# Performance work log

Measured on AMD Instinct MI355X. Metric: run time of the kernel, lower is better.

Reference implementation:

```python
import jax, jax.numpy as jnp
import numpy as np

MARGIN = 0.0
GAP = 0.4
N, D, C = 8192, 128, 10


def setup_inputs() -> dict:
    key = jax.random.key(0)
    k1, k2, k3 = jax.random.split(key, 3)
    inputs = jax.random.normal(k1, (N, D), dtype=jnp.float32)
    pred = jax.random.normal(k2, (N, C), dtype=jnp.float32)
    targets = jax.random.randint(k3, (N,), 0, C, dtype=jnp.int64)
    return {"inputs": inputs, "pred": pred, "targets": targets}


def reference(inputs, pred, targets):
    n = inputs.shape[0]
    # pairwise euclidean distances: ||xi||^2 + ||xj||^2 - 2 xi.xj, clamped + sqrt
    sq = jnp.sum(inputs * inputs, axis=1)                      # [n]
    dist = sq[:, None] + sq[None, :] - 2.0 * (inputs @ inputs.T)
    dist = jnp.sqrt(jnp.clip(dist, 1e-12))                     # [n, n]
    same = targets[:, None] == targets[None, :]                # [n, n] bool

    # confusion detection (original runs under no_grad)
    p = jax.nn.softmax(jax.lax.stop_gradient(pred), axis=1)
    val, top2 = jax.lax.top_k(p, 2)                            # [n,2]
    confuse = (val[:, 0] - val[:, 1] <= GAP) | (top2[:, 0] != targets)  # [n]

    # hard mining per row: hardest positive (max over same-class), hardest negative (min over diff-class)
    dist_ap = jnp.max(jnp.where(same, dist, -jnp.inf), axis=1)  # [n]
    dist_an = jnp.min(jnp.where(same, jnp.inf, dist), axis=1)   # [n]

    # MarginRankingLoss(margin=MARGIN) with y=1: mean(relu(-(an - ap) + margin)) over confused rows
    per_row = jnp.maximum(dist_ap - dist_an + MARGIN, 0.0)
    cnt = jnp.sum(confuse.astype(jnp.float32))
    loss = jnp.sum(jnp.where(confuse, per_row, 0.0)) / jnp.maximum(cnt, 1.0)
    return jnp.where(cnt > 0, loss, 0.0)
```

## Files before the change

kernel.cpp:

```cpp
#include <hip/hip_runtime.h>

#define NROWS 8192
#define DIMX  128
#define DIM2  160
#define NCLS  10
#define GAPV  0.4f
#define BIAS  2048.0f
#define C0    128.0f
#define CHUNK 512
#define NJ    (CHUNK / 16)

typedef __attribute__((ext_vector_type(8))) short bf16x8;
typedef __attribute__((ext_vector_type(4))) float f32x4;

__device__ __forceinline__ unsigned fenc(float f) {
  unsigned u = __float_as_uint(f);
  return (u & 0x80000000u) ? ~u : (u | 0x80000000u);
}
__device__ __forceinline__ float fdec(unsigned u) {
  return (u & 0x80000000u) ? __uint_as_float(u & 0x7fffffffu) : __uint_as_float(~u);
}
__device__ __forceinline__ short f2bf(float f) {
  unsigned u = __float_as_uint(f);
  u += 0x7fffu + ((u >> 16) & 1u);
  return (short)(u >> 16);
}

__global__ __launch_bounds__(256) void prep_k(const float* __restrict__ x,
                                              const int* __restrict__ tgt,
                                              const float* __restrict__ pred,
                                              short* __restrict__ xa,
                                              short* __restrict__ xbm,
                                              float* __restrict__ sq,
                                              unsigned* __restrict__ emax,
                                              unsigned* __restrict__ emin,
                                              int* __restrict__ conf) {
  const int wave = threadIdx.x >> 6;
  const int lane = threadIdx.x & 63;
  const int row  = blockIdx.x * 4 + wave;
  const float* p = x + (size_t)row * DIMX;
  const float a = p[lane];
  const float b = p[lane + 64];
  float s = a * a + b * b;
  #pragma unroll
  for (int m = 1; m < 64; m <<= 1) s += __shfl_xor(s, m, 64);

  short* pa = xa  + (size_t)row * DIM2;
  short* pb = xbm + (size_t)row * DIM2;
  pa[lane] = f2bf(a); pa[lane + 64] = f2bf(b);
  pb[lane] = f2bf(a); pb[lane + 64] = f2bf(b);

  const int cls = tgt[row];
  if (lane < 32) {
    short va, vb;
    if (lane == 0)          { va = (short)0x3F80; vb = f2bf(-0.5f * (s - C0)); }
    else if (lane <= NCLS)  { const bool hit = (lane - 1) == cls;
                              va = hit ? (short)0x4200 : (short)0;
                              vb = hit ? (short)0xC200 : (short)0; }
    else                    { va = 0; vb = 0; }
    pa[128 + lane] = va;
    pb[128 + lane] = vb;
  }

  if (lane == 0) {
    sq[row]   = s;
    emax[row] = fenc(-INFINITY);
    emin[row] = fenc(INFINITY);
    const float* pp = pred + (size_t)row * NCLS;
    float v[NCLS];
    #pragma unroll
    for (int c = 0; c < NCLS; ++c) v[c] = pp[c];
    float m1 = v[0]; int i1 = 0;
    #pragma unroll
    for (int c = 1; c < NCLS; ++c)
      if (v[c] > m1) { m1 = v[c]; i1 = c; }
    float m2 = -INFINITY, sum = 0.f;
    #pragma unroll
    for (int c = 0; c < NCLS; ++c) {
      sum += __expf(v[c] - m1);
      if (c != i1) m2 = fmaxf(m2, v[c]);
    }
    const float d01 = (1.f - __expf(m2 - m1)) / sum;
    conf[row] = (d01 <= GAPV) || (i1 != cls);
  }
}

__global__ __launch_bounds__(64, 2) void gram_k(const short* __restrict__ xa,
                                                const short* __restrict__ xbm,
                                                unsigned* __restrict__ emax,
                                                unsigned* __restrict__ emin) {
  const int lane = threadIdx.x;
  const int quad = lane >> 4;
  const int m16  = lane & 15;
  const int i0    = blockIdx.x * 64;
  const int jbase = blockIdx.y * CHUNK;

  bf16x8 A[4][5];
  #pragma unroll
  for (int r = 0; r < 4; ++r) {
    const short* pa = xa + (size_t)(i0 + r * 16 + m16) * DIM2 + quad * 8;
    #pragma unroll
    for (int ks = 0; ks < 5; ++ks)
      A[r][ks] = *(const bf16x8*)(pa + ks * 32);
  }

  float gmin[4][4], gmax[4][4];
  #pragma unroll
  for (int r = 0; r < 4; ++r)
    #pragma unroll
    for (int q = 0; q < 4; ++q) { gmin[r][q] = INFINITY; gmax[r][q] = -INFINITY; }

  const short* pb0 = xbm + (size_t)(jbase + m16) * DIM2 + quad * 8;
  bf16x8 Bc[5];
  #pragma unroll
  for (int ks = 0; ks < 5; ++ks) Bc[ks] = *(const bf16x8*)(pb0 + ks * 32);

  #pragma unroll 2
  for (int jt = 0; jt < NJ; ++jt) {
    const short* pn = pb0 + (size_t)((jt + 1 < NJ) ? (jt + 1) * 16 : 0) * DIM2;
    bf16x8 Bn[5];
    #pragma unroll
    for (int ks = 0; ks < 5; ++ks) Bn[ks] = *(const bf16x8*)(pn + ks * 32);

    f32x4 acc[4];
    #pragma unroll
    for (int r = 0; r < 4; ++r) acc[r] = (f32x4){0.f, 0.f, 0.f, 0.f};
    #pragma unroll
    for (int ks = 0; ks < 5; ++ks)
      #pragma unroll
      for (int r = 0; r < 4; ++r)
        acc[r] = __builtin_amdgcn_mfma_f32_16x16x32_bf16(A[r][ks], Bc[ks], acc[r], 0, 0, 0);

    #pragma unroll
    for (int r = 0; r < 4; ++r)
      #pragma unroll
      for (int q = 0; q < 4; ++q) {
        gmin[r][q] = fminf(gmin[r][q], acc[r][q]);
        gmax[r][q] = fmaxf(gmax[r][q], acc[r][q]);
      }

    #pragma unroll
    for (int ks = 0; ks < 5; ++ks) Bc[ks] = Bn[ks];
  }

  #pragma unroll
  for (int m = 1; m <= 8; m <<= 1)
    #pragma unroll
    for (int r = 0; r < 4; ++r)
      #pragma unroll
      for (int q = 0; q < 4; ++q) {
        gmin[r][q] = fminf(gmin[r][q], __shfl_xor(gmin[r][q], m, 64));
        gmax[r][q] = fmaxf(gmax[r][q], __shfl_xor(gmax[r][q], m, 64));
      }

  if (m16 == 0) {
    #pragma unroll
    for (int r = 0; r < 4; ++r)
      #pragma unroll
      for (int q = 0; q < 4; ++q) {
        const int row = i0 + r * 16 + quad * 4 + q;
        atomicMax(&emax[row], fenc(C0 - 2.f * gmin[r][q] - BIAS));
        atomicMin(&emin[row], fenc(C0 - 2.f * gmax[r][q]));
      }
  }
}

__global__ __launch_bounds__(1024) void finalize_k(const float* __restrict__ sq,
                                                   const unsigned* __restrict__ emax,
                                                   const unsigned* __restrict__ emin,
                                                   const int* __restrict__ conf,
                                                   float* __restrict__ out) {
  float s = 0.f, c = 0.f;
  for (int row = threadIdx.x; row < NROWS; row += 1024) {
    if (conf[row]) {
      const float ap = sqrtf(fmaxf(sq[row] + fdec(emax[row]), 1e-12f));
      const float an = sqrtf(fmaxf(sq[row] + fdec(emin[row]), 1e-12f));
      s += fmaxf(ap - an, 0.f);
      c += 1.f;
    }
  }
  #pragma unroll
  for (int m = 1; m < 64; m <<= 1) {
    s += __shfl_xor(s, m, 64);
    c += __shfl_xor(c, m, 64);
  }
  __shared__ float ss[16], cc[16];
  const int wid = threadIdx.x >> 6;
  if ((threadIdx.x & 63) == 0) { ss[wid] = s; cc[wid] = c; }
  __syncthreads();
  if (threadIdx.x == 0) {
    float S = 0.f, C = 0.f;
    for (int w = 0; w < 16; ++w) { S += ss[w]; C += cc[w]; }
    out[0] = (C > 0.f) ? (S / fmaxf(C, 1.f)) : 0.f;
  }
}

extern "C" void kernel_launch(void* const* d_in, const int* in_sizes, int n_in,
                              void* d_out, int out_size, void* d_ws, size_t ws_size,
                              hipStream_t stream) {
  const float* x    = (const float*)d_in[0];
  const float* pred = (const float*)d_in[1];
  const int*   tgt  = (const int*)d_in[2];
  float* out = (float*)d_out;

  char* w = (char*)d_ws;
  const size_t arr_bytes = (size_t)NROWS * DIM2 * 2;
  short*    xa   = (short*)w;
  short*    xbm  = (short*)(w + arr_bytes);
  float*    sq   = (float*)(w + 2 * arr_bytes);
  unsigned* emax = (unsigned*)(w + 2 * arr_bytes + (size_t)NROWS * 4);
  unsigned* emin = (unsigned*)(w + 2 * arr_bytes + (size_t)NROWS * 8);
  int*      conf = (int*)(w + 2 * arr_bytes + (size_t)NROWS * 12);

  hipLaunchKernelGGL(prep_k, dim3(NROWS / 4), dim3(256), 0, stream,
                     x, tgt, pred, xa, xbm, sq, emax, emin, conf);
  hipLaunchKernelGGL(gram_k, dim3(NROWS / 64, NROWS / CHUNK), dim3(64), 0, stream,
                     xa, xbm, emax, emin);
  hipLaunchKernelGGL(finalize_k, dim3(1), dim3(1024), 0, stream,
                     sq, emax, emin, conf, out);
}
```

Measured before the change: 99.70 us.

## Share B tiles across four waves via double-buffered LDS staging in gram kernel

```diff
diff --git a/kernel.cpp b/kernel.cpp
--- a/kernel.cpp
+++ b/kernel.cpp
@@ -8,7 +8,9 @@
 #define BIAS  2048.0f
 #define C0    128.0f
 #define CHUNK 512
-#define NJ    (CHUNK / 16)
+#define SLAB  32
+#define NSLAB (CHUNK / SLAB)
+#define LDST  168
 
 typedef __attribute__((ext_vector_type(8))) short bf16x8;
 typedef __attribute__((ext_vector_type(4))) float f32x4;
@@ -85,14 +87,17 @@
   }
 }
 
-__global__ __launch_bounds__(64, 2) void gram_k(const short* __restrict__ xa,
-                                                const short* __restrict__ xbm,
-                                                unsigned* __restrict__ emax,
-                                                unsigned* __restrict__ emin) {
-  const int lane = threadIdx.x;
+__global__ __launch_bounds__(256, 2) void gram_k(const short* __restrict__ xa,
+                                                 const short* __restrict__ xbm,
+                                                 unsigned* __restrict__ emax,
+                                                 unsigned* __restrict__ emin) {
+  __shared__ short lds[2][SLAB * LDST];
+  const int tid  = threadIdx.x;
+  const int wave = tid >> 6;
+  const int lane = tid & 63;
   const int quad = lane >> 4;
   const int m16  = lane & 15;
-  const int i0    = blockIdx.x * 64;
+  const int i0    = blockIdx.x * 256 + wave * 64;
   const int jbase = blockIdx.y * CHUNK;
 
   bf16x8 A[4][5];
@@ -110,37 +115,53 @@
     #pragma unroll
     for (int q = 0; q < 4; ++q) { gmin[r][q] = INFINITY; gmax[r][q] = -INFINITY; }
 
-  const short* pb0 = xbm + (size_t)(jbase + m16) * DIM2 + quad * 8;
-  bf16x8 Bc[5];
-  #pragma unroll
-  for (int ks = 0; ks < 5; ++ks) Bc[ks] = *(const bf16x8*)(pb0 + ks * 32);
-
-  #pragma unroll 2
-  for (int jt = 0; jt < NJ; ++jt) {
-    const short* pn = pb0 + (size_t)((jt + 1 < NJ) ? (jt + 1) * 16 : 0) * DIM2;
-    bf16x8 Bn[5];
-    #pragma unroll
-    for (int ks = 0; ks < 5; ++ks) Bn[ks] = *(const bf16x8*)(pn + ks * 32);
-
-    f32x4 acc[4];
-    #pragma unroll
-    for (int r = 0; r < 4; ++r) acc[r] = (f32x4){0.f, 0.f, 0.f, 0.f};
-    #pragma unroll
-    for (int ks = 0; ks < 5; ++ks)
+  const int scol = tid >> 3;
+  const int sseg = tid & 3 ? (tid & 7) : (tid & 7);
+  uint2 st[5];
+  {
+    const short* g0 = xbm + (size_t)(jbase + scol) * DIM2 + (tid & 7) * 4;
+    #pragma unroll
+    for (int u = 0; u < 5; ++u) st[u] = *(const uint2*)(g0 + u * 32);
+  }
+
+  for (int s = 0; s < NSLAB; ++s) {
+    short* buf = lds[s & 1];
+    {
+      short* dst = buf + scol * LDST + (tid & 7) * 4;
+      #pragma unroll
+      for (int u = 0; u < 5; ++u) *(uint2*)(dst + u * 32) = st[u];
+    }
+    if (s + 1 < NSLAB) {
+      const short* gn = xbm + (size_t)(jbase + (s + 1) * SLAB + scol) * DIM2 + (tid & 7) * 4;
+      #pragma unroll
+      for (int u = 0; u < 5; ++u) st[u] = *(const uint2*)(gn + u * 32);
+    }
+    __syncthreads();
+
+    #pragma unroll
+    for (int jt = 0; jt < SLAB / 16; ++jt) {
+      const short* pb = buf + (jt * 16 + m16) * LDST + quad * 8;
+      bf16x8 B[5];
+      #pragma unroll
+      for (int ks = 0; ks < 5; ++ks) B[ks] = *(const bf16x8*)(pb + ks * 32);
+
+      f32x4 acc[4];
+      #pragma unroll
+      for (int r = 0; r < 4; ++r) acc[r] = (f32x4){0.f, 0.f, 0.f, 0.f};
+      #pragma unroll
+      for (int ks = 0; ks < 5; ++ks)
+        #pragma unroll
+        for (int r = 0; r < 4; ++r)
+          acc[r] = __builtin_amdgcn_mfma_f32_16x16x32_bf16(A[r][ks], B[ks], acc[r], 0, 0, 0);
+
       #pragma unroll
       for (int r = 0; r < 4; ++r)
-        acc[r] = __builtin_amdgcn_mfma_f32_16x16x32_bf16(A[r][ks], Bc[ks], acc[r], 0, 0, 0);
-
-    #pragma unroll
-    for (int r = 0; r < 4; ++r)
-      #pragma unroll
-      for (int q = 0; q < 4; ++q) {
-        gmin[r][q] = fminf(gmin[r][q], acc[r][q]);
-        gmax[r][q] = fmaxf(gmax[r][q], acc[r][q]);
-      }
-
-    #pragma unroll
-    for (int ks = 0; ks < 5; ++ks) Bc[ks] = Bn[ks];
+        #pragma unroll
+        for (int q = 0; q < 4; ++q) {
+          gmin[r][q] = fminf(gmin[r][q], acc[r][q]);
+          gmax[r][q] = fmaxf(gmax[r][q], acc[r][q]);
+        }
+    }
   }
 
   #pragma unroll
@@ -214,7 +235,7 @@
 
   hipLaunchKernelGGL(prep_k, dim3(NROWS / 4), dim3(256), 0, stream,
                      x, tgt, pred, xa, xbm, sq, emax, emin, conf);
-  hipLaunchKernelGGL(gram_k, dim3(NROWS / 64, NROWS / CHUNK), dim3(64), 0, stream,
+  hipLaunchKernelGGL(gram_k, dim3(NROWS / 256, NROWS / CHUNK), dim3(256), 0, stream,
                      xa, xbm, emax, emin);
   hipLaunchKernelGGL(finalize_k, dim3(1), dim3(1024), 0, stream,
                      sq, emax, emin, conf, out);
```

Result: faster. 93.16 us (-6.6%).
